# Optimization experiments

Measured on AMD Instinct MI355X. Metric: run time of the kernel, lower is better.

## Reference

```python
import jax, jax.numpy as jnp
import numpy as np

N_NODES = 50000
N_EDGES = 600000
IN_C = 128
HID = 128
OUT_C = 32
N_GRAPHS = 64


def setup_inputs() -> dict:
    key = jax.random.key(0)
    ks = jax.random.split(key, 12)
    x = jax.random.normal(ks[0], (N_NODES, IN_C), dtype=jnp.float32)
    edge_index = jax.random.randint(ks[1], (2, N_EDGES), 0, N_NODES, dtype=jnp.int64)
    batch = jnp.sort(jax.random.randint(ks[2], (N_NODES,), 0, N_GRAPHS, dtype=jnp.int64))
    s1 = 1.0 / np.sqrt(IN_C)
    s2 = 1.0 / np.sqrt(HID)
    # SAGEConv: out = lin_l(mean_neighbors) + lin_r(x); lin_l has bias, lin_r has none
    W1l = jax.random.uniform(ks[3], (HID, IN_C), minval=-s1, maxval=s1, dtype=jnp.float32)
    b1 = jax.random.uniform(ks[4], (HID,), minval=-s1, maxval=s1, dtype=jnp.float32)
    W1r = jax.random.uniform(ks[5], (HID, IN_C), minval=-s1, maxval=s1, dtype=jnp.float32)
    W2l = jax.random.uniform(ks[6], (HID, HID), minval=-s2, maxval=s2, dtype=jnp.float32)
    b2 = jax.random.uniform(ks[7], (HID,), minval=-s2, maxval=s2, dtype=jnp.float32)
    W2r = jax.random.uniform(ks[8], (HID, HID), minval=-s2, maxval=s2, dtype=jnp.float32)
    Wlin = jax.random.uniform(ks[9], (OUT_C, HID), minval=-s2, maxval=s2, dtype=jnp.float32)
    blin = jax.random.uniform(ks[10], (OUT_C,), minval=-s2, maxval=s2, dtype=jnp.float32)
    return {"x": x, "edge_index": edge_index, "batch": batch,
            "W1l": W1l, "b1": b1, "W1r": W1r,
            "W2l": W2l, "b2": b2, "W2r": W2r,
            "Wlin": Wlin, "blin": blin}


def _sage_conv(x, src, dst, Wl, bl, Wr):
    # mean aggregation of source-node features onto destination nodes
    msg_sum = jax.ops.segment_sum(x[src], dst, num_segments=N_NODES)  # [N, d]
    deg = jax.ops.segment_sum(jnp.ones((src.shape[0],), x.dtype), dst, num_segments=N_NODES)
    mean = msg_sum / jnp.maximum(deg, 1.0)[:, None]
    return mean @ Wl.T + bl + x @ Wr.T


def reference(x, edge_index, batch, W1l, b1, W1r, W2l, b2, W2r, Wlin, blin):
    src, dst = edge_index[0], edge_index[1]
    h = jax.nn.relu(_sage_conv(x, src, dst, W1l, b1, W1r))
    h = jax.nn.relu(_sage_conv(h, src, dst, W2l, b2, W2r))
    # global mean pool over graph ids
    gsum = jax.ops.segment_sum(h, batch, num_segments=N_GRAPHS)        # [G, HID]
    cnt = jax.ops.segment_sum(jnp.ones((h.shape[0],), h.dtype), batch, num_segments=N_GRAPHS)
    pooled = gsum / jnp.maximum(cnt, 1.0)[:, None]
    return pooled @ Wlin.T + blin
```

## Files before the change

kernel.cpp:

```cpp
#include <hip/hip_runtime.h>
#include <hip/hip_fp16.h>

#define N_NODES 50000
#define N_EDGES 600000
#define N_GRAPHS 64
#define HID 128
#define OUT_C 32

#define N_SCAN_BLOCKS ((N_NODES + 255) / 256)
#define SCAN_FLAG 0x40000000

typedef __attribute__((ext_vector_type(8))) _Float16 half8;
typedef __attribute__((ext_vector_type(4))) float f32x4;

#define ZERO_INTS (2 * N_NODES + N_SCAN_BLOCKS)

__global__ __launch_bounds__(256) void zero_kernel(int* __restrict__ zb) {
    int i = blockIdx.x * 256 + threadIdx.x;
    if (i < ZERO_INTS) zb[i] = 0;
}

#define DEG_BLOCKS ((N_EDGES + 255) / 256)
#define GST_BLOCKS ((N_NODES + 256) / 256)

__global__ __launch_bounds__(256) void deg_gst_w(
    const int* __restrict__ dst, int* __restrict__ degi,
    const int* __restrict__ batch, int* __restrict__ gstart,
    const float* __restrict__ W1l, const float* __restrict__ W1r,
    const float* __restrict__ W2l, const float* __restrict__ W2r,
    __half* __restrict__ Wt1, __half* __restrict__ Wt2) {
    const int b = blockIdx.x;
    const int t = threadIdx.x;
    if (b < DEG_BLOCKS) {
        int e = b * 256 + t;
        if (e < N_EDGES) atomicAdd(&degi[dst[e]], 1);
    } else if (b < DEG_BLOCKS + GST_BLOCKS) {
        int i = (b - DEG_BLOCKS) * 256 + t;
        if (i <= N_NODES) {
            if (i == 0) {
                int b1 = batch[0];
                for (int g = 0; g <= b1; ++g) gstart[g] = 0;
            } else if (i == N_NODES) {
                int b0 = batch[N_NODES - 1];
                for (int g = b0 + 1; g <= N_GRAPHS; ++g) gstart[g] = N_NODES;
            } else {
                int b0 = batch[i - 1], b1 = batch[i];
                for (int g = b0 + 1; g <= b1; ++g) gstart[g] = i;
            }
        }
    } else {
        int local = (b - DEG_BLOCKS - GST_BLOCKS) * 256 + t;
        for (int i = local; i < 65536; i += 4096) {
            int which = i >> 15;
            int j = i & 32767;
            int n = j >> 8, k = j & 255;
            const float* Wl = which ? W2l : W1l;
            const float* Wr = which ? W2r : W1r;
            float a = (k < 128) ? Wl[n * 128 + k] : Wr[n * 128 + (k - 128)];
            (which ? Wt2 : Wt1)[j] = __float2half(a);
        }
    }
}

__global__ __launch_bounds__(256) void scan_fused(
    const int* __restrict__ deg, int* __restrict__ bsum,
    int* __restrict__ rowptr, float* __restrict__ invdeg) {
    __shared__ int s[256];
    const int b = blockIdx.x;
    const int t = threadIdx.x;
    const int idx = b * 256 + t;
    const int v = (idx < N_NODES) ? deg[idx] : 0;
    s[t] = v;
    __syncthreads();
    for (int off = 1; off < 256; off <<= 1) {
        int u = (t >= off) ? s[t - off] : 0;
        __syncthreads();
        s[t] += u;
        __syncthreads();
    }
    const int incl = s[t];
    if (t == 255) atomicExch(&bsum[b], incl | SCAN_FLAG);

    int pv = 0;
    if (t < b) {
        int w;
        do { w = atomicAdd(&bsum[t], 0); } while (!(w & SCAN_FLAG));
        pv = w & ~SCAN_FLAG;
    }
    __syncthreads();
    s[t] = pv;
    __syncthreads();
    for (int off = 128; off > 0; off >>= 1) {
        if (t < off) s[t] += s[t + off];
        __syncthreads();
    }
    const int boffs = s[0];

    if (idx < N_NODES) {
        rowptr[idx] = boffs + incl - v;
        invdeg[idx] = 1.0f / fmaxf((float)v, 1.0f);
    }
    if (b == N_SCAN_BLOCKS - 1 && t == 255) rowptr[N_NODES] = boffs + incl;
}

__global__ __launch_bounds__(256) void fill_cast(
    const int* __restrict__ src, const int* __restrict__ dst,
    const int* __restrict__ rowptr, int* __restrict__ cursor,
    int* __restrict__ eidx,
    const float* __restrict__ x, __half* __restrict__ xh) {
    const int b = blockIdx.x;
    const int t = threadIdx.x;
    if (b < DEG_BLOCKS) {
        int e = b * 256 + t;
        if (e < N_EDGES) {
            int d = dst[e];
            int pos = atomicAdd(&cursor[d], 1);
            eidx[rowptr[d] + pos] = src[e];
        }
    } else {
        int i = ((b - DEG_BLOCKS) * 256 + t) * 4;
        if (i < N_NODES * 128) {
            float4 v = *(const float4*)(x + i);
            __half2 a = __floats2half2_rn(v.x, v.y);
            __half2 c = __floats2half2_rn(v.z, v.w);
            uint2 st;
            st.x = *(const unsigned int*)&a;
            st.y = *(const unsigned int*)&c;
            *(uint2*)(xh + i) = st;
        }
    }
}

__global__ __launch_bounds__(256) void aggregate_f16(
    const __half* __restrict__ feat16, const int* __restrict__ rowptr,
    const int* __restrict__ eidx, const float* __restrict__ invdeg,
    __half* __restrict__ mean16) {
    const int tid  = threadIdx.x;
    const int lane = tid & 63;
    const int sub  = lane & 15;
    const int gbase = lane & 48;
    const int node = blockIdx.x * 16 + (tid >> 4);
    const bool act = (node < N_NODES);
    int beg = 0, end = 0;
    if (act) { beg = rowptr[node]; end = rowptr[node + 1]; }
    const int deg = end - beg;
    const size_t coff = (size_t)sub * 8;

    int pre0 = 0, pre1 = 0;
    if (deg > 0) {
        pre0 = eidx[min(beg + sub,      end - 1)];
        pre1 = eidx[min(beg + 16 + sub, end - 1)];
    }

    float4 a[4], bb[4];
#pragma unroll
    for (int g = 0; g < 4; ++g) { a[g] = (float4){0.f,0.f,0.f,0.f}; bb[g] = (float4){0.f,0.f,0.f,0.f}; }

    for (int j0 = 0; j0 < deg; j0 += 16) {
        int idx[16];
        if (j0 == 0) {
#pragma unroll
            for (int k = 0; k < 16; ++k) idx[k] = __shfl(pre0, gbase + k);
        } else if (j0 == 16) {
#pragma unroll
            for (int k = 0; k < 16; ++k) idx[k] = __shfl(pre1, gbase + k);
        } else {
#pragma unroll
            for (int k = 0; k < 16; ++k) idx[k] = eidx[min(beg + j0 + k, end - 1)];
        }
        half8 v[16];
#pragma unroll
        for (int k = 0; k < 16; ++k)
            v[k] = *(const half8*)(feat16 + (size_t)idx[k] * 128 + coff);
        const int rem = deg - j0;
#pragma unroll
        for (int k = 0; k < 16; ++k) {
            const float w = (k < rem) ? 1.0f : 0.0f;
            const int g = k & 3;
            a[g].x  += w * (float)v[k][0];
            a[g].y  += w * (float)v[k][1];
            a[g].z  += w * (float)v[k][2];
            a[g].w  += w * (float)v[k][3];
            bb[g].x += w * (float)v[k][4];
            bb[g].y += w * (float)v[k][5];
            bb[g].z += w * (float)v[k][6];
            bb[g].w += w * (float)v[k][7];
        }
    }

    if (act) {
        const float sc = invdeg[node];
        half8 r;
        r[0] = (_Float16)(((a[0].x + a[1].x) + (a[2].x + a[3].x)) * sc);
        r[1] = (_Float16)(((a[0].y + a[1].y) + (a[2].y + a[3].y)) * sc);
        r[2] = (_Float16)(((a[0].z + a[1].z) + (a[2].z + a[3].z)) * sc);
        r[3] = (_Float16)(((a[0].w + a[1].w) + (a[2].w + a[3].w)) * sc);
        r[4] = (_Float16)(((bb[0].x + bb[1].x) + (bb[2].x + bb[3].x)) * sc);
        r[5] = (_Float16)(((bb[0].y + bb[1].y) + (bb[2].y + bb[3].y)) * sc);
        r[6] = (_Float16)(((bb[0].z + bb[1].z) + (bb[2].z + bb[3].z)) * sc);
        r[7] = (_Float16)(((bb[0].w + bb[1].w) + (bb[2].w + bb[3].w)) * sc);
        *(half8*)(mean16 + (size_t)node * 128 + coff) = r;
    }
}

#define GBM 64
#define BPAD 8

__global__ __launch_bounds__(256) void sage_gemm_f16(
    const __half* __restrict__ mean16, const __half* __restrict__ feat16,
    const __half* __restrict__ Wt, const float* __restrict__ bias,
    __half* __restrict__ out16, int M) {
    __shared__ __align__(16) __half Bs[128][256 + BPAD];

    const int tid = threadIdx.x;
    const int wave = tid >> 6;
    const int lane = tid & 63;
    const int l15 = lane & 15;
    const int quad = lane >> 4;
    const int row0 = blockIdx.x * GBM;
    const int gi_a = min(row0 + wave * 16 + l15, M - 1);

    for (int id = tid; id < 128 * 32; id += 256) {
        int n = id >> 5;
        int kc = (id & 31) * 8;
        *(half8*)&Bs[n][kc] = *(const half8*)(Wt + (size_t)n * 256 + kc);
    }

    half8 af[8];
#pragma unroll
    for (int kb = 0; kb < 8; ++kb) {
        const int k0 = kb * 32;
        const __half* ap = (k0 < 128)
            ? (mean16 + (size_t)gi_a * 128 + k0 + quad * 8)
            : (feat16 + (size_t)gi_a * 128 + (k0 - 128) + quad * 8);
        af[kb] = *(const half8*)ap;
    }

    f32x4 acc[8];
#pragma unroll
    for (int t = 0; t < 8; ++t) acc[t] = (f32x4){0.f, 0.f, 0.f, 0.f};

    __syncthreads();

#pragma unroll
    for (int kb = 0; kb < 8; ++kb) {
#pragma unroll
        for (int t = 0; t < 8; ++t) {
            const half8 b = *(const half8*)&Bs[t * 16 + l15][kb * 32 + quad * 8];
            acc[t] = __builtin_amdgcn_mfma_f32_16x16x32_f16(af[kb], b, acc[t], 0, 0, 0);
        }
    }

#pragma unroll
    for (int r = 0; r < 4; ++r) {
        int gi = row0 + wave * 16 + quad * 4 + r;
        if (gi < M) {
#pragma unroll
            for (int t = 0; t < 8; ++t) {
                int col = t * 16 + l15;
                float v = fmaxf(acc[t][r] + bias[col], 0.f);
                out16[(size_t)gi * 128 + col] = __float2half(v);
            }
        }
    }
}

#define POOL_PARTS 4
__global__ __launch_bounds__(256) void pool_parts(
    const __half* __restrict__ h, const int* __restrict__ gstart,
    float* __restrict__ pooled_parts) {
    const int g = blockIdx.x >> 2;
    const int part = blockIdx.x & 3;
    const int start = gstart[g];
    const int end = gstart[g + 1];

    const int t = threadIdx.x;
    const int c4 = (t & 31) * 4;
    const int rg = t >> 5;
    float4 acc = {0.f, 0.f, 0.f, 0.f};
    for (int n = start + part * 8 + rg; n < end; n += 8 * POOL_PARTS) {
        const __half2* p = (const __half2*)(h + (size_t)n * 128 + c4);
        float2 f0 = __half22float2(p[0]);
        float2 f1 = __half22float2(p[1]);
        acc.x += f0.x; acc.y += f0.y; acc.z += f1.x; acc.w += f1.y;
    }
    __shared__ float sm[8][132];
    sm[rg][c4 + 0] = acc.x;
    sm[rg][c4 + 1] = acc.y;
    sm[rg][c4 + 2] = acc.z;
    sm[rg][c4 + 3] = acc.w;
    __syncthreads();
    if (t < 128) {
        float s = 0.f;
#pragma unroll
        for (int r = 0; r < 8; ++r) s += sm[r][t];
        pooled_parts[(size_t)blockIdx.x * 128 + t] = s;
    }
}

__global__ void final_kernel(const float* __restrict__ pooled_parts,
                             const int* __restrict__ gstart,
                             const float* __restrict__ Wlin, const float* __restrict__ blin,
                             float* __restrict__ out) {
    int g = blockIdx.x;
    int j = threadIdx.x;
    float inv = 1.0f / fmaxf((float)(gstart[g + 1] - gstart[g]), 1.0f);
    float sum = blin[j];
    const float* w = Wlin + j * 128;
    const float* p0 = pooled_parts + (size_t)(g * 4 + 0) * 128;
    const float* p1 = pooled_parts + (size_t)(g * 4 + 1) * 128;
    const float* p2 = pooled_parts + (size_t)(g * 4 + 2) * 128;
    const float* p3 = pooled_parts + (size_t)(g * 4 + 3) * 128;
    for (int c = 0; c < 128; ++c) {
        float p = (p0[c] + p1[c]) + (p2[c] + p3[c]);
        sum += p * inv * w[c];
    }
    out[g * 32 + j] = sum;
}

extern "C" void kernel_launch(void* const* d_in, const int* in_sizes, int n_in,
                              void* d_out, int out_size, void* d_ws, size_t ws_size,
                              hipStream_t stream) {
    const float* x    = (const float*)d_in[0];
    const int*   src  = (const int*)d_in[1];
    const int*   dst  = ((const int*)d_in[1]) + N_EDGES;
    const int*   batch= (const int*)d_in[2];
    const float* W1l  = (const float*)d_in[3];
    const float* b1   = (const float*)d_in[4];
    const float* W1r  = (const float*)d_in[5];
    const float* W2l  = (const float*)d_in[6];
    const float* b2   = (const float*)d_in[7];
    const float* W2r  = (const float*)d_in[8];
    const float* Wlin = (const float*)d_in[9];
    const float* blin = (const float*)d_in[10];
    float* out = (float*)d_out;

    __half* xh     = (__half*)d_ws;
    __half* mean16 = xh + 6400000;
    __half* h1_16  = mean16 + 6400000;
    __half* h2_16  = h1_16 + 6400000;
    __half* Wt1    = h2_16 + 6400000;
    __half* Wt2    = Wt1 + 32768;
    float* pooled_parts = (float*)(Wt2 + 32768);
    float* invdeg  = pooled_parts + 32768;
    int*   gstart  = (int*)(invdeg + N_NODES);
    int*   degi    = gstart + 65;
    int*   cursor  = degi + N_NODES;
    int*   bsum    = cursor + N_NODES;
    int*   rowptr  = bsum + N_SCAN_BLOCKS;
    int*   eidx    = rowptr + N_NODES + 1;

    zero_kernel<<<(ZERO_INTS + 255) / 256, 256, 0, stream>>>(degi);

    deg_gst_w<<<DEG_BLOCKS + GST_BLOCKS + 16, 256, 0, stream>>>(
        dst, degi, batch, gstart, W1l, W1r, W2l, W2r, Wt1, Wt2);

    scan_fused<<<N_SCAN_BLOCKS, 256, 0, stream>>>(degi, bsum, rowptr, invdeg);

    fill_cast<<<DEG_BLOCKS + (N_NODES * 128 / 4 + 255) / 256, 256, 0, stream>>>(
        src, dst, rowptr, cursor, eidx, x, xh);

    const int gemm_grid = (N_NODES + GBM - 1) / GBM;
    const int agg_grid = (N_NODES + 15) / 16;

    aggregate_f16<<<agg_grid, 256, 0, stream>>>(xh, rowptr, eidx, invdeg, mean16);
    sage_gemm_f16<<<gemm_grid, 256, 0, stream>>>(mean16, xh, Wt1, b1, h1_16, N_NODES);

    aggregate_f16<<<agg_grid, 256, 0, stream>>>(h1_16, rowptr, eidx, invdeg, mean16);
    sage_gemm_f16<<<gemm_grid, 256, 0, stream>>>(mean16, h1_16, Wt2, b2, h2_16, N_NODES);

    pool_parts<<<N_GRAPHS * POOL_PARTS, 256, 0, stream>>>(h2_16, gstart, pooled_parts);
    final_kernel<<<N_GRAPHS, 32, 0, stream>>>(pooled_parts, gstart, Wlin, blin, out);
}
```

Measured before the change: 252.0 us.

## Fuse neighbor aggregation, SAGE GEMM and global mean pooling into one kernel

Merges each layer's aggregation and GEMM into one kernel: the block gathers 64 node means into swizzled LDS and feeds them straight to MFMA, so the mean16 round trip through global memory goes away. In the second layer it also reduces pooled sums per graph inside the block with atomics, removing the h2 store and the separate pooling kernel. The weight LDS layout moves from padding to XOR swizzling. The cost is 80KB LDS per block, which limits occupancy, and each block now does both a serial gather and the GEMM, so the two phases no longer overlap across kernels.

```diff
diff --git a/kernel.cpp b/kernel.cpp
--- a/kernel.cpp
+++ b/kernel.cpp
@@ -13,7 +13,7 @@
 typedef __attribute__((ext_vector_type(8))) _Float16 half8;
 typedef __attribute__((ext_vector_type(4))) float f32x4;
 
-#define ZERO_INTS (2 * N_NODES + N_SCAN_BLOCKS)
+#define ZERO_INTS (2 * N_NODES + N_SCAN_BLOCKS + N_GRAPHS * HID)
 
 __global__ __launch_bounds__(256) void zero_kernel(int* __restrict__ zb) {
     int i = blockIdx.x * 256 + threadIdx.x;
@@ -131,65 +131,96 @@
     }
 }
 
-__global__ __launch_bounds__(256) void aggregate_f16(
+#define GBM 64
+
+__global__ __launch_bounds__(256, 2) void sage_fused(
     const __half* __restrict__ feat16, const int* __restrict__ rowptr,
     const int* __restrict__ eidx, const float* __restrict__ invdeg,
-    __half* __restrict__ mean16) {
-    const int tid  = threadIdx.x;
+    const __half* __restrict__ Wt, const float* __restrict__ bias,
+    __half* __restrict__ out16,
+    const int* __restrict__ batch, float* __restrict__ pooled,
+    int M, int do_pool) {
+    __shared__ __align__(16) __half Bs[128 * 256];
+    __shared__ __align__(16) __half Ms[64 * 128];
+
+    const int tid = threadIdx.x;
+    const int wave = tid >> 6;
     const int lane = tid & 63;
-    const int sub  = lane & 15;
+    const int l15 = lane & 15;
+    const int quad = lane >> 4;
+    const int row0 = blockIdx.x * GBM;
+
+    for (int id = tid; id < 128 * 32; id += 256) {
+        int n = id >> 5;
+        int kc16 = (id & 31) * 16;
+        int off = (n * 512 + kc16) ^ ((n & 7) << 4);
+        *(half8*)((char*)Bs + off) = *(const half8*)((const char*)Wt + n * 512 + kc16);
+    }
+
+    const int g16 = tid >> 4;
+    const int sub = tid & 15;
     const int gbase = lane & 48;
-    const int node = blockIdx.x * 16 + (tid >> 4);
-    const bool act = (node < N_NODES);
-    int beg = 0, end = 0;
-    if (act) { beg = rowptr[node]; end = rowptr[node + 1]; }
-    const int deg = end - beg;
     const size_t coff = (size_t)sub * 8;
 
-    int pre0 = 0, pre1 = 0;
-    if (deg > 0) {
-        pre0 = eidx[min(beg + sub,      end - 1)];
-        pre1 = eidx[min(beg + 16 + sub, end - 1)];
-    }
-
-    float4 a[4], bb[4];
-#pragma unroll
-    for (int g = 0; g < 4; ++g) { a[g] = (float4){0.f,0.f,0.f,0.f}; bb[g] = (float4){0.f,0.f,0.f,0.f}; }
-
-    for (int j0 = 0; j0 < deg; j0 += 16) {
-        int idx[16];
-        if (j0 == 0) {
-#pragma unroll
-            for (int k = 0; k < 16; ++k) idx[k] = __shfl(pre0, gbase + k);
-        } else if (j0 == 16) {
-#pragma unroll
-            for (int k = 0; k < 16; ++k) idx[k] = __shfl(pre1, gbase + k);
-        } else {
-#pragma unroll
-            for (int k = 0; k < 16; ++k) idx[k] = eidx[min(beg + j0 + k, end - 1)];
-        }
-        half8 v[16];
-#pragma unroll
-        for (int k = 0; k < 16; ++k)
-            v[k] = *(const half8*)(feat16 + (size_t)idx[k] * 128 + coff);
-        const int rem = deg - j0;
-#pragma unroll
-        for (int k = 0; k < 16; ++k) {
-            const float w = (k < rem) ? 1.0f : 0.0f;
-            const int g = k & 3;
-            a[g].x  += w * (float)v[k][0];
-            a[g].y  += w * (float)v[k][1];
-            a[g].z  += w * (float)v[k][2];
-            a[g].w  += w * (float)v[k][3];
-            bb[g].x += w * (float)v[k][4];
-            bb[g].y += w * (float)v[k][5];
-            bb[g].z += w * (float)v[k][6];
-            bb[g].w += w * (float)v[k][7];
-        }
-    }
-
-    if (act) {
-        const float sc = invdeg[node];
+    int begq[4], endq[4], pre0q[4], pre1q[4];
+#pragma unroll
+    for (int q = 0; q < 4; ++q) {
+        int node = row0 + g16 + 16 * q;
+        int bq = 0, eq = 0;
+        if (node < M) { bq = rowptr[node]; eq = rowptr[node + 1]; }
+        begq[q] = bq; endq[q] = eq;
+    }
+#pragma unroll
+    for (int q = 0; q < 4; ++q) {
+        int bq = begq[q], eq = endq[q];
+        pre0q[q] = (eq > bq) ? eidx[min(bq + sub,      eq - 1)] : 0;
+        pre1q[q] = (eq > bq) ? eidx[min(bq + 16 + sub, eq - 1)] : 0;
+    }
+
+#pragma unroll
+    for (int q = 0; q < 4; ++q) {
+        const int nloc = g16 + 16 * q;
+        const int node = row0 + nloc;
+        const int beg = begq[q], end = endq[q];
+        const int deg = end - beg;
+
+        float4 a[4], bb[4];
+#pragma unroll
+        for (int g = 0; g < 4; ++g) { a[g] = (float4){0.f,0.f,0.f,0.f}; bb[g] = (float4){0.f,0.f,0.f,0.f}; }
+
+        for (int j0 = 0; j0 < deg; j0 += 16) {
+            int idx[16];
+            if (j0 == 0) {
+#pragma unroll
+                for (int k = 0; k < 16; ++k) idx[k] = __shfl(pre0q[q], gbase + k);
+            } else if (j0 == 16) {
+#pragma unroll
+                for (int k = 0; k < 16; ++k) idx[k] = __shfl(pre1q[q], gbase + k);
+            } else {
+#pragma unroll
+                for (int k = 0; k < 16; ++k) idx[k] = eidx[min(beg + j0 + k, end - 1)];
+            }
+            half8 v[16];
+#pragma unroll
+            for (int k = 0; k < 16; ++k)
+                v[k] = *(const half8*)(feat16 + (size_t)idx[k] * 128 + coff);
+            const int rem = deg - j0;
+#pragma unroll
+            for (int k = 0; k < 16; ++k) {
+                const float w = (k < rem) ? 1.0f : 0.0f;
+                const int g = k & 3;
+                a[g].x  += w * (float)v[k][0];
+                a[g].y  += w * (float)v[k][1];
+                a[g].z  += w * (float)v[k][2];
+                a[g].w  += w * (float)v[k][3];
+                bb[g].x += w * (float)v[k][4];
+                bb[g].y += w * (float)v[k][5];
+                bb[g].z += w * (float)v[k][6];
+                bb[g].w += w * (float)v[k][7];
+            }
+        }
+
+        const float sc = (node < M) ? invdeg[node] : 1.0f;
         half8 r;
         r[0] = (_Float16)(((a[0].x + a[1].x) + (a[2].x + a[3].x)) * sc);
         r[1] = (_Float16)(((a[0].y + a[1].y) + (a[2].y + a[3].y)) * sc);
@@ -199,106 +230,88 @@
         r[5] = (_Float16)(((bb[0].y + bb[1].y) + (bb[2].y + bb[3].y)) * sc);
         r[6] = (_Float16)(((bb[0].z + bb[1].z) + (bb[2].z + bb[3].z)) * sc);
         r[7] = (_Float16)(((bb[0].w + bb[1].w) + (bb[2].w + bb[3].w)) * sc);
-        *(half8*)(mean16 + (size_t)node * 128 + coff) = r;
-    }
-}
-
-#define GBM 64
-#define BPAD 8
-
-__global__ __launch_bounds__(256) void sage_gemm_f16(
-    const __half* __restrict__ mean16, const __half* __restrict__ feat16,
-    const __half* __restrict__ Wt, const float* __restrict__ bias,
-    __half* __restrict__ out16, int M) {
-    __shared__ __align__(16) __half Bs[128][256 + BPAD];
-
-    const int tid = threadIdx.x;
-    const int wave = tid >> 6;
-    const int lane = tid & 63;
-    const int l15 = lane & 15;
-    const int quad = lane >> 4;
-    const int row0 = blockIdx.x * GBM;
-    const int gi_a = min(row0 + wave * 16 + l15, M - 1);
-
-    for (int id = tid; id < 128 * 32; id += 256) {
-        int n = id >> 5;
-        int kc = (id & 31) * 8;
-        *(half8*)&Bs[n][kc] = *(const half8*)(Wt + (size_t)n * 256 + kc);
-    }
-
+        int moff = (nloc * 256 + (int)sub * 16) ^ ((nloc & 7) << 4);
+        *(half8*)((char*)Ms + moff) = r;
+    }
+
+    __syncthreads();
+
+    const int arow = wave * 16 + l15;
+    const int gi_a = min(row0 + arow, M - 1);
     half8 af[8];
 #pragma unroll
+    for (int kb = 0; kb < 4; ++kb) {
+        int off = (arow * 256 + kb * 64 + quad * 16) ^ ((arow & 7) << 4);
+        af[kb] = *(const half8*)((const char*)Ms + off);
+    }
+#pragma unroll
+    for (int kb = 4; kb < 8; ++kb) {
+        af[kb] = *(const half8*)(feat16 + (size_t)gi_a * 128 + (kb - 4) * 32 + quad * 8);
+    }
+
+    f32x4 acc[8];
+#pragma unroll
+    for (int t = 0; t < 8; ++t) acc[t] = (f32x4){0.f, 0.f, 0.f, 0.f};
+
+#pragma unroll
     for (int kb = 0; kb < 8; ++kb) {
-        const int k0 = kb * 32;
-        const __half* ap = (k0 < 128)
-            ? (mean16 + (size_t)gi_a * 128 + k0 + quad * 8)
-            : (feat16 + (size_t)gi_a * 128 + (k0 - 128) + quad * 8);
-        af[kb] = *(const half8*)ap;
-    }
-
-    f32x4 acc[8];
-#pragma unroll
-    for (int t = 0; t < 8; ++t) acc[t] = (f32x4){0.f, 0.f, 0.f, 0.f};
-
-    __syncthreads();
-
-#pragma unroll
-    for (int kb = 0; kb < 8; ++kb) {
 #pragma unroll
         for (int t = 0; t < 8; ++t) {
-            const half8 b = *(const half8*)&Bs[t * 16 + l15][kb * 32 + quad * 8];
+            const int n = t * 16 + l15;
+            const int boff = (n * 512 + kb * 64 + quad * 16) ^ ((n & 7) << 4);
+            const half8 b = *(const half8*)((const char*)Bs + boff);
             acc[t] = __builtin_amdgcn_mfma_f32_16x16x32_f16(af[kb], b, acc[t], 0, 0, 0);
         }
     }
 
-#pragma unroll
-    for (int r = 0; r < 4; ++r) {
-        int gi = row0 + wave * 16 + quad * 4 + r;
-        if (gi < M) {
+    if (!do_pool) {
+#pragma unroll
+        for (int r = 0; r < 4; ++r) {
+            int gi = row0 + wave * 16 + quad * 4 + r;
+            if (gi < M) {
+#pragma unroll
+                for (int t = 0; t < 8; ++t) {
+                    int col = t * 16 + l15;
+                    float v = fmaxf(acc[t][r] + bias[col], 0.f);
+                    out16[(size_t)gi * 128 + col] = __float2half(v);
+                }
+            }
+        }
+    } else {
+        __syncthreads();
+#pragma unroll
+        for (int r = 0; r < 4; ++r) {
+            int lrow = wave * 16 + quad * 4 + r;
+            int gi = row0 + lrow;
 #pragma unroll
             for (int t = 0; t < 8; ++t) {
                 int col = t * 16 + l15;
                 float v = fmaxf(acc[t][r] + bias[col], 0.f);
-                out16[(size_t)gi * 128 + col] = __float2half(v);
-            }
-        }
-    }
-}
-
-#define POOL_PARTS 4
-__global__ __launch_bounds__(256) void pool_parts(
-    const __half* __restrict__ h, const int* __restrict__ gstart,
-    float* __restrict__ pooled_parts) {
-    const int g = blockIdx.x >> 2;
-    const int part = blockIdx.x & 3;
-    const int start = gstart[g];
-    const int end = gstart[g + 1];
-
-    const int t = threadIdx.x;
-    const int c4 = (t & 31) * 4;
-    const int rg = t >> 5;
-    float4 acc = {0.f, 0.f, 0.f, 0.f};
-    for (int n = start + part * 8 + rg; n < end; n += 8 * POOL_PARTS) {
-        const __half2* p = (const __half2*)(h + (size_t)n * 128 + c4);
-        float2 f0 = __half22float2(p[0]);
-        float2 f1 = __half22float2(p[1]);
-        acc.x += f0.x; acc.y += f0.y; acc.z += f1.x; acc.w += f1.y;
-    }
-    __shared__ float sm[8][132];
-    sm[rg][c4 + 0] = acc.x;
-    sm[rg][c4 + 1] = acc.y;
-    sm[rg][c4 + 2] = acc.z;
-    sm[rg][c4 + 3] = acc.w;
-    __syncthreads();
-    if (t < 128) {
-        float s = 0.f;
-#pragma unroll
-        for (int r = 0; r < 8; ++r) s += sm[r][t];
-        pooled_parts[(size_t)blockIdx.x * 128 + t] = s;
-    }
-}
-
-__global__ void final_kernel(const float* __restrict__ pooled_parts,
+                if (gi >= M) v = 0.f;
+                int off = (lrow * 256 + col * 2) ^ ((lrow & 7) << 4);
+                *(__half*)((char*)Ms + off) = __float2half(v);
+            }
+        }
+        __syncthreads();
+        if (tid < 128) {
+            const int col = tid;
+            int cur = batch[min(row0, M - 1)];
+            float s = 0.f;
+            for (int r = 0; r < 64; ++r) {
+                int gr = batch[min(row0 + r, M - 1)];
+                if (gr != cur) {
+                    atomicAdd(&pooled[cur * 128 + col], s);
+                    s = 0.f; cur = gr;
+                }
+                int off = (r * 256 + col * 2) ^ ((r & 7) << 4);
+                s += __half2float(*(const __half*)((const char*)Ms + off));
+            }
+            atomicAdd(&pooled[cur * 128 + col], s);
+        }
+    }
+}
+
+__global__ void final_kernel(const float* __restrict__ pooled,
                              const int* __restrict__ gstart,
                              const float* __restrict__ Wlin, const float* __restrict__ blin,
                              float* __restrict__ out) {
@@ -307,13 +320,9 @@
     float inv = 1.0f / fmaxf((float)(gstart[g + 1] - gstart[g]), 1.0f);
     float sum = blin[j];
     const float* w = Wlin + j * 128;
-    const float* p0 = pooled_parts + (size_t)(g * 4 + 0) * 128;
-    const float* p1 = pooled_parts + (size_t)(g * 4 + 1) * 128;
-    const float* p2 = pooled_parts + (size_t)(g * 4 + 2) * 128;
-    const float* p3 = pooled_parts + (size_t)(g * 4 + 3) * 128;
+    const float* p = pooled + (size_t)g * 128;
     for (int c = 0; c < 128; ++c) {
-        float p = (p0[c] + p1[c]) + (p2[c] + p3[c]);
-        sum += p * inv * w[c];
+        sum += p[c] * inv * w[c];
     }
     out[g * 32 + j] = sum;
 }
@@ -336,18 +345,16 @@
     float* out = (float*)d_out;
 
     __half* xh     = (__half*)d_ws;
-    __half* mean16 = xh + 6400000;
-    __half* h1_16  = mean16 + 6400000;
-    __half* h2_16  = h1_16 + 6400000;
-    __half* Wt1    = h2_16 + 6400000;
+    __half* h1_16  = xh + 6400000;
+    __half* Wt1    = h1_16 + 6400000;
     __half* Wt2    = Wt1 + 32768;
-    float* pooled_parts = (float*)(Wt2 + 32768);
-    float* invdeg  = pooled_parts + 32768;
+    float* invdeg  = (float*)(Wt2 + 32768);
     int*   gstart  = (int*)(invdeg + N_NODES);
     int*   degi    = gstart + 65;
     int*   cursor  = degi + N_NODES;
     int*   bsum    = cursor + N_NODES;
-    int*   rowptr  = bsum + N_SCAN_BLOCKS;
+    float* pooled  = (float*)(bsum + N_SCAN_BLOCKS);
+    int*   rowptr  = (int*)(pooled + N_GRAPHS*HID);
     int*   eidx    = rowptr + N_NODES + 1;
 
     zero_kernel<<<(ZERO_INTS + 255) / 256, 256, 0, stream>>>(degi);
@@ -360,15 +367,13 @@
     fill_cast<<<DEG_BLOCKS + (N_NODES * 128 / 4 + 255) / 256, 256, 0, stream>>>(
         src, dst, rowptr, cursor, eidx, x, xh);
 
-    const int gemm_grid = (N_NODES + GBM - 1) / GBM;
-    const int agg_grid = (N_NODES + 15) / 16;
-
-    aggregate_f16<<<agg_grid, 256, 0, stream>>>(xh, rowptr, eidx, invdeg, mean16);
-    sage_gemm_f16<<<gemm_grid, 256, 0, stream>>>(mean16, xh, Wt1, b1, h1_16, N_NODES);
-
-    aggregate_f16<<<agg_grid, 256, 0, stream>>>(h1_16, rowptr, eidx, invdeg, mean16);
-    sage_gemm_f16<<<gemm_grid, 256, 0, stream>>>(mean16, h1_16, Wt2, b2, h2_16, N_NODES);
-
-    pool_parts<<<N_GRAPHS * POOL_PARTS, 256, 0, stream>>>(h2_16, gstart, pooled_parts);
-    final_kernel<<<N_GRAPHS, 32, 0, stream>>>(pooled_parts, gstart, Wlin, blin, out);
-}
+    const int grid = (N_NODES + GBM - 1) / GBM;
+
+    sage_fused<<<grid, 256, 0, stream>>>(
+        xh, rowptr, eidx, invdeg, Wt1, b1, h1_16, batch, pooled, N_NODES, 0);
+
+    sage_fused<<<grid, 256, 0, stream>>>(
+        h1_16, rowptr, eidx, invdeg, Wt2, b2, (__half*)0, batch, pooled, N_NODES, 1);
+
+    final_kernel<<<N_GRAPHS, 32, 0, stream>>>(pooled, gstart, Wlin, blin, out);
+}
```

After: 250.5 us. Within noise of the previous version (-0.6%).
